# Optimization experiments

Hardware: AMD Instinct MI355X
Metric: run time of the kernel (lower is better)

The kernel has to match this reference:

```python
import math
import jax, jax.numpy as jnp
import numpy as np

DIM_Q = 1024
DIM_K = 1024
DIM_V = 1024
NUM_HEADS = 16
B, NQ, NK = 4, 1024, 1024
LN_EPS = 1e-5


def setup_inputs() -> dict:
    key = jax.random.key(0)
    ks = jax.random.split(key, 16)
    s = lambda fan_in: 1.0 / math.sqrt(fan_in)
    inp = {
        "Q": jax.random.normal(ks[0], (B, NQ, DIM_Q), dtype=jnp.float32),
        "K": jax.random.normal(ks[1], (B, NK, DIM_K), dtype=jnp.float32),
        # attention projections (nn.Linear: weight [out, in])
        "Wq": jax.random.uniform(ks[2], (DIM_V, DIM_Q), jnp.float32, -s(DIM_Q), s(DIM_Q)),
        "bq": jax.random.uniform(ks[3], (DIM_V,), jnp.float32, -s(DIM_Q), s(DIM_Q)),
        "Wk": jax.random.uniform(ks[4], (DIM_V, DIM_K), jnp.float32, -s(DIM_K), s(DIM_K)),
        "bk": jax.random.uniform(ks[5], (DIM_V,), jnp.float32, -s(DIM_K), s(DIM_K)),
        "Wv": jax.random.uniform(ks[6], (DIM_V, DIM_K), jnp.float32, -s(DIM_K), s(DIM_K)),
        "bv": jax.random.uniform(ks[7], (DIM_V,), jnp.float32, -s(DIM_K), s(DIM_K)),
        # LayerNorms
        "ln0_g": jnp.ones((DIM_V,), jnp.float32),
        "ln0_b": jnp.zeros((DIM_V,), jnp.float32),
        "ln1_g": jnp.ones((DIM_V,), jnp.float32),
        "ln1_b": jnp.zeros((DIM_V,), jnp.float32),
        # SwiGLU: w12 [2*hidden, in], w3 [out, hidden], hidden = out = DIM_V
        "W12": jax.random.uniform(ks[8], (2 * DIM_V, DIM_V), jnp.float32, -s(DIM_V), s(DIM_V)),
        "b12": jax.random.uniform(ks[9], (2 * DIM_V,), jnp.float32, -s(DIM_V), s(DIM_V)),
        "W3": jax.random.uniform(ks[10], (DIM_V, DIM_V), jnp.float32, -s(DIM_V), s(DIM_V)),
        "b3": jax.random.uniform(ks[11], (DIM_V,), jnp.float32, -s(DIM_V), s(DIM_V)),
    }
    return inp


def _layernorm(x, g, b):
    mu = jnp.mean(x, axis=-1, keepdims=True)
    var = jnp.mean(jnp.square(x - mu), axis=-1, keepdims=True)
    return (x - mu) * jax.lax.rsqrt(var + LN_EPS) * g + b


def reference(Q, K, Wq, bq, Wk, bk, Wv, bv, ln0_g, ln0_b, ln1_g, ln1_b, W12, b12, W3, b3):
    H = NUM_HEADS
    dh = DIM_V // H
    Qp = jnp.einsum("bnd,vd->bnv", Q, Wq) + bq   # [B,NQ,DIM_V]
    Kp = jnp.einsum("bnd,vd->bnv", K, Wk) + bk   # [B,NK,DIM_V]
    Vp = jnp.einsum("bnd,vd->bnv", K, Wv) + bv
    # torch.cat(x.split(dh, 2), 0) => layout [H*B, N, dh] with head index major
    Qh = Qp.reshape(B, NQ, H, dh).transpose(2, 0, 1, 3)  # [H,B,NQ,dh]
    Kh = Kp.reshape(B, NK, H, dh).transpose(2, 0, 1, 3)
    Vh = Vp.reshape(B, NK, H, dh).transpose(2, 0, 1, 3)
    # NOTE: original scales by sqrt(dim_V), not sqrt(head_dim)
    scores = jnp.einsum("hbqd,hbkd->hbqk", Qh, Kh) / math.sqrt(DIM_V)
    A = jax.nn.softmax(scores, axis=-1)                  # [H,B,NQ,NK]
    Oh = Qh + jnp.einsum("hbqk,hbkd->hbqd", A, Vh)       # residual pre-concat
    O = Oh.transpose(1, 2, 0, 3).reshape(B, NQ, DIM_V)
    O = _layernorm(O, ln0_g, ln0_b)
    # SwiGLU FFN
    x12 = jnp.einsum("bnd,hd->bnh", O, W12) + b12
    x1, x2 = jnp.split(x12, 2, axis=-1)
    O = O + (jnp.einsum("bnh,oh->bno", jax.nn.silu(x1) * x2, W3) + b3)
    O = _layernorm(O, ln1_g, ln1_b)
    return O, A.reshape(H * B, NQ, NK)
```

## Files before the change

### kernel.cpp

```cpp
#include <hip/hip_runtime.h>
#include <math.h>

#define BATCH 4
#define NQL   1024
#define NKL   1024
#define DIM   1024
#define NHEAD 16
#define DHEAD 64
#define SCALE 0.03125f

typedef float  f32x4  __attribute__((ext_vector_type(4)));
typedef short  short8 __attribute__((ext_vector_type(8)));

__device__ __forceinline__ ushort f2bf(float x) {
    uint u = __float_as_uint(x);
    u += 0x7FFFu + ((u >> 16) & 1u);
    return (ushort)(u >> 16);
}
__device__ __forceinline__ float bf2f(ushort h) {
    return __uint_as_float(((uint)h) << 16);
}

__global__ __launch_bounds__(256)
void split_bf(const float* __restrict__ x, ushort* __restrict__ hi,
              ushort* __restrict__ lo, int n4)
{
    const int i = blockIdx.x * 256 + threadIdx.x;
    if (i >= n4) return;
    const float4 v = ((const float4*)x)[i];
    ushort4 h, l;
    h.x = f2bf(v.x); l.x = f2bf(v.x - bf2f(h.x));
    h.y = f2bf(v.y); l.y = f2bf(v.y - bf2f(h.y));
    h.z = f2bf(v.z); l.z = f2bf(v.z - bf2f(h.z));
    h.w = f2bf(v.w); l.w = f2bf(v.w - bf2f(h.w));
    ((ushort4*)hi)[i] = h;
    ((ushort4*)lo)[i] = l;
}

#define LDK 40

template<int NPROD, int BIAS, int RESID, int OMODE>
__global__ __launch_bounds__(256)
void gemm_mfma(const ushort* __restrict__ Ahi, const ushort* __restrict__ Alo,
               int lda,
               const ushort* __restrict__ Bhi, const ushort* __restrict__ Blo,
               int ldb,
               const float* __restrict__ bias,
               const float* __restrict__ rm,
               float* __restrict__ Cm, ushort* __restrict__ Chi,
               int ldc, int Kd, float scale)
{
    constexpr int NT_ = (NPROD == 3) ? 4 : 2;
    __shared__ ushort lds[2][NT_][128 * LDK];

    const int tid  = threadIdx.x;
    const int lane = tid & 63;
    const int wid  = tid >> 6;
    const int wr   = wid >> 1, wc = wid & 1;
    const int bm   = blockIdx.x * 128;
    const int bn   = blockIdx.y * 128;

    const ushort* tb[NT_];
    int tldv[NT_];
    tb[0] = Ahi + (size_t)bm * lda;  tldv[0] = lda;
    tb[1] = Bhi + (size_t)bn * ldb;  tldv[1] = ldb;
    if constexpr (NPROD == 3) {
        tb[2] = Alo + (size_t)bm * lda;  tldv[2] = lda;
        tb[3] = Blo + (size_t)bn * ldb;  tldv[3] = ldb;
    }

    int4 rg[NT_][2];
    auto gload = [&](int k0) {
#pragma unroll
        for (int tt = 0; tt < NT_; ++tt)
#pragma unroll
            for (int p = 0; p < 2; ++p) {
                const int idx = p * 256 + tid;
                rg[tt][p] = *(const int4*)(tb[tt] + (size_t)(idx >> 2) * tldv[tt]
                                           + k0 + ((idx & 3) << 3));
            }
    };
    auto dswrite = [&](int buf) {
#pragma unroll
        for (int tt = 0; tt < NT_; ++tt)
#pragma unroll
            for (int p = 0; p < 2; ++p) {
                const int idx = p * 256 + tid;
                *(int4*)&lds[buf][tt][(idx >> 2) * LDK + ((idx & 3) << 3)] = rg[tt][p];
            }
    };

    gload(0);
    dswrite(0);
    __syncthreads();

    f32x4 acc[4][4] = {};
    int cur = 0;
    const int nt = Kd >> 5;

    const int rA = wr * 64 + (lane & 15);
    const int rB = wc * 64 + (lane & 15);
    const int kg = (lane >> 4) << 3;

    for (int t = 0; t < nt; ++t) {
        const bool more = (t + 1) < nt;
        if (more) gload((t + 1) << 5);

        short8 ah[4], bh[4], al[4], bl[4];
#pragma unroll
        for (int f = 0; f < 4; ++f) {
            ah[f] = *(const short8*)&lds[cur][0][(rA + f * 16) * LDK + kg];
            bh[f] = *(const short8*)&lds[cur][1][(rB + f * 16) * LDK + kg];
        }
        if constexpr (NPROD == 3) {
#pragma unroll
            for (int f = 0; f < 4; ++f) {
                al[f] = *(const short8*)&lds[cur][2][(rA + f * 16) * LDK + kg];
                bl[f] = *(const short8*)&lds[cur][3][(rB + f * 16) * LDK + kg];
            }
        }

#pragma unroll
        for (int fi = 0; fi < 4; ++fi)
#pragma unroll
            for (int fj = 0; fj < 4; ++fj) {
                acc[fi][fj] = __builtin_amdgcn_mfma_f32_16x16x32_bf16(ah[fi], bh[fj], acc[fi][fj], 0, 0, 0);
                if constexpr (NPROD == 3) {
                    acc[fi][fj] = __builtin_amdgcn_mfma_f32_16x16x32_bf16(ah[fi], bl[fj], acc[fi][fj], 0, 0, 0);
                    acc[fi][fj] = __builtin_amdgcn_mfma_f32_16x16x32_bf16(al[fi], bh[fj], acc[fi][fj], 0, 0, 0);
                }
            }

        if (more) dswrite(cur ^ 1);
        __syncthreads();
        cur ^= 1;
    }

    float biasv[4];
    if (BIAS) {
#pragma unroll
        for (int fj = 0; fj < 4; ++fj)
            biasv[fj] = bias[bn + wc * 64 + fj * 16 + (lane & 15)];
    }
#pragma unroll
    for (int fi = 0; fi < 4; ++fi) {
        const int r0 = bm + wr * 64 + fi * 16 + ((lane >> 4) << 2);
#pragma unroll
        for (int fj = 0; fj < 4; ++fj) {
            const int c = bn + wc * 64 + fj * 16 + (lane & 15);
            if constexpr (OMODE == 3) {
                ushort4 v4;
#pragma unroll
                for (int r = 0; r < 4; ++r) {
                    float o = acc[fi][fj][r] * scale;
                    if (BIAS) o += biasv[fj];
                    ((ushort*)&v4)[r] = f2bf(o);
                }
                const int b   = r0 >> 10;
                const int key = r0 & 1023;
                const int h   = c >> 6;
                const int d   = c & 63;
                *(ushort4*)(Chi + ((size_t)((h << 2) + b) << 16) + (size_t)d * 1024 + key) = v4;
            } else {
#pragma unroll
                for (int r = 0; r < 4; ++r) {
                    float o = acc[fi][fj][r] * scale;
                    if (BIAS) o += biasv[fj];
                    if (RESID) o += rm[(size_t)(r0 + r) * ldc + c];
                    if (OMODE == 0 || OMODE == 1)
                        Cm[(size_t)(r0 + r) * ldc + c] = o;
                    if (OMODE == 1 || OMODE == 2)
                        Chi[(size_t)(r0 + r) * ldc + c] = f2bf(o);
                }
            }
        }
    }
}

__global__ __launch_bounds__(256)
void flash_attn(const ushort* __restrict__ QpHi,
                const ushort* __restrict__ KpHi,
                const ushort* __restrict__ Vt,
                const float*  __restrict__ Qp,
                float* __restrict__ Aout,
                float* __restrict__ Oa)
{
    __shared__ ushort Ks[2][64][72];
    __shared__ ushort Vs[2][64][72];
    __shared__ ushort Ps[4][32][72];

    const int tid  = threadIdx.x;
    const int lane = tid & 63;
    const int w    = tid >> 6;
    const int l15  = lane & 15;
    const int lg   = lane >> 4;
    const int bm   = blockIdx.x * 128;
    const int hb   = blockIdx.y;
    const int zh   = hb >> 2, zb = hb & 3;

    const ushort* Qb  = QpHi + ((size_t)zb << 20) + zh * 64;
    const ushort* Kb  = KpHi + ((size_t)zb << 20) + zh * 64;
    const ushort* Vtb = Vt   + ((size_t)hb << 16);
    const float*  Qrb = Qp   + ((size_t)zb << 20) + zh * 64 + (size_t)bm * DIM;
    float* Ab = Aout + ((size_t)hb << 20) + (size_t)bm * NKL;
    float* Ob = Oa   + ((size_t)zb << 20) + zh * 64 + (size_t)bm * DIM;

    short8 qf[2][2];
#pragma unroll
    for (int qg = 0; qg < 2; ++qg)
#pragma unroll
        for (int kg = 0; kg < 2; ++kg)
            qf[qg][kg] = *(const short8*)(Qb + (size_t)(bm + w * 32 + qg * 16 + l15) * DIM
                                          + kg * 32 + lg * 8);

    int4 kreg[2], vreg[2];
    auto kload = [&](int kt) {
#pragma unroll
        for (int p = 0; p < 2; ++p) {
            const int c = p * 256 + tid;
            kreg[p] = *(const int4*)(Kb + (size_t)(kt * 64 + (c >> 3)) * DIM + (c & 7) * 8);
        }
    };
    auto kstore = [&](int buf) {
#pragma unroll
        for (int p = 0; p < 2; ++p) {
            const int c = p * 256 + tid;
            *(int4*)&Ks[buf][c >> 3][(c & 7) * 8] = kreg[p];
        }
    };
    auto vload = [&](int kt) {
#pragma unroll
        for (int p = 0; p < 2; ++p) {
            const int c = p * 256 + tid;
            vreg[p] = *(const int4*)(Vtb + (size_t)(c >> 3) * 1024 + kt * 64 + (c & 7) * 8);
        }
    };
    auto vstore = [&](int buf) {
#pragma unroll
        for (int p = 0; p < 2; ++p) {
            const int c = p * 256 + tid;
            *(int4*)&Vs[buf][c >> 3][(c & 7) * 8] = vreg[p];
        }
    };
    auto qk = [&](int buf, f32x4 (*s)[4]) {
        short8 kf[4][2];
#pragma unroll
        for (int cg = 0; cg < 4; ++cg)
#pragma unroll
            for (int kg = 0; kg < 2; ++kg)
                kf[cg][kg] = *(const short8*)&Ks[buf][cg * 16 + l15][kg * 32 + lg * 8];
#pragma unroll
        for (int qg = 0; qg < 2; ++qg)
#pragma unroll
            for (int cg = 0; cg < 4; ++cg) {
                s[qg][cg] = __builtin_amdgcn_mfma_f32_16x16x32_bf16(qf[qg][0], kf[cg][0], s[qg][cg], 0, 0, 0);
                s[qg][cg] = __builtin_amdgcn_mfma_f32_16x16x32_bf16(qf[qg][1], kf[cg][1], s[qg][cg], 0, 0, 0);
            }
    };

    float mrun[2][4], lrun[2][4];
#pragma unroll
    for (int qg = 0; qg < 2; ++qg)
#pragma unroll
        for (int r = 0; r < 4; ++r) { mrun[qg][r] = -INFINITY; lrun[qg][r] = 0.f; }

    kload(0); kstore(0); __syncthreads();
    for (int kt = 0; kt < 16; ++kt) {
        const bool more = kt < 15;
        if (more) kload(kt + 1);
        f32x4 s[2][4] = {};
        qk(kt & 1, s);
#pragma unroll
        for (int qg = 0; qg < 2; ++qg)
#pragma unroll
            for (int r = 0; r < 4; ++r) {
                const float v0 = s[qg][0][r] * SCALE, v1 = s[qg][1][r] * SCALE;
                const float v2 = s[qg][2][r] * SCALE, v3 = s[qg][3][r] * SCALE;
                const float tm = fmaxf(fmaxf(v0, v1), fmaxf(v2, v3));
                const float mn = fmaxf(mrun[qg][r], tm);
                const float sc = __expf(mrun[qg][r] - mn);
                lrun[qg][r] = lrun[qg][r] * sc
                            + __expf(v0 - mn) + __expf(v1 - mn)
                            + __expf(v2 - mn) + __expf(v3 - mn);
                mrun[qg][r] = mn;
            }
        if (more) { kstore((kt + 1) & 1); __syncthreads(); }
    }

    float mf[2][4], li[2][4];
#pragma unroll
    for (int qg = 0; qg < 2; ++qg)
#pragma unroll
        for (int r = 0; r < 4; ++r) {
            float m = mrun[qg][r];
#pragma unroll
            for (int off = 1; off < 16; off <<= 1) m = fmaxf(m, __shfl_xor(m, off));
            float lv = lrun[qg][r] * __expf(mrun[qg][r] - m);
#pragma unroll
            for (int off = 1; off < 16; off <<= 1) lv += __shfl_xor(lv, off);
            mf[qg][r] = m;
            li[qg][r] = 1.f / lv;
        }

    kload(0); vload(0);
    __syncthreads();
    kstore(0); vstore(0);
    __syncthreads();

    f32x4 oacc[2][4] = {};
    for (int kt = 0; kt < 16; ++kt) {
        const bool more = kt < 15;
        if (more) { kload(kt + 1); vload(kt + 1); }
        f32x4 s[2][4] = {};
        qk(kt & 1, s);

#pragma unroll
        for (int qg = 0; qg < 2; ++qg)
#pragma unroll
            for (int cg = 0; cg < 4; ++cg) {
#pragma unroll
                for (int r = 0; r < 4; ++r) {
                    const float p = __expf(s[qg][cg][r] * SCALE - mf[qg][r]) * li[qg][r];
                    Ps[w][qg * 16 + lg * 4 + r][cg * 16 + l15] = f2bf(p);
                    Ab[(size_t)(w * 32 + qg * 16 + lg * 4 + r) * NKL
                       + kt * 64 + cg * 16 + l15] = p;
                }
            }

        short8 pf[2][2], vf[4][2];
#pragma unroll
        for (int qg = 0; qg < 2; ++qg)
#pragma unroll
            for (int kk = 0; kk < 2; ++kk)
                pf[qg][kk] = *(const short8*)&Ps[w][qg * 16 + l15][kk * 32 + lg * 8];
#pragma unroll
        for (int dg = 0; dg < 4; ++dg)
#pragma unroll
            for (int kk = 0; kk < 2; ++kk)
                vf[dg][kk] = *(const short8*)&Vs[kt & 1][dg * 16 + l15][kk * 32 + lg * 8];
#pragma unroll
        for (int qg = 0; qg < 2; ++qg)
#pragma unroll
            for (int dg = 0; dg < 4; ++dg) {
                oacc[qg][dg] = __builtin_amdgcn_mfma_f32_16x16x32_bf16(pf[qg][0], vf[dg][0], oacc[qg][dg], 0, 0, 0);
                oacc[qg][dg] = __builtin_amdgcn_mfma_f32_16x16x32_bf16(pf[qg][1], vf[dg][1], oacc[qg][dg], 0, 0, 0);
            }

        if (more) { kstore((kt + 1) & 1); vstore((kt + 1) & 1); __syncthreads(); }
    }

#pragma unroll
    for (int qg = 0; qg < 2; ++qg)
#pragma unroll
        for (int dg = 0; dg < 4; ++dg)
#pragma unroll
            for (int r = 0; r < 4; ++r) {
                const size_t idx = (size_t)(w * 32 + qg * 16 + lg * 4 + r) * DIM
                                 + dg * 16 + l15;
                Ob[idx] = oacc[qg][dg][r] + Qrb[idx];
            }
}

template<int SPLIT>
__global__ __launch_bounds__(256)
void ln_rows(const float* __restrict__ in, const float* __restrict__ g,
             const float* __restrict__ b, float* __restrict__ out,
             ushort* __restrict__ ohi, ushort* __restrict__ olo)
{
    const int row = blockIdx.x;
    const int tid = threadIdx.x;
    const float4 xv = *(const float4*)(in + (size_t)row * DIM + (tid << 2));

    float s = xv.x + xv.y + xv.z + xv.w;
    float q = xv.x * xv.x + xv.y * xv.y + xv.z * xv.z + xv.w * xv.w;
#pragma unroll
    for (int off = 32; off; off >>= 1) {
        s += __shfl_xor(s, off);
        q += __shfl_xor(q, off);
    }
    __shared__ float ss[4], qq[4];
    if ((tid & 63) == 0) { ss[tid >> 6] = s; qq[tid >> 6] = q; }
    __syncthreads();
    s = ss[0] + ss[1] + ss[2] + ss[3];
    q = qq[0] + qq[1] + qq[2] + qq[3];

    const float mu  = s * (1.f / 1024.f);
    const float var = q * (1.f / 1024.f) - mu * mu;
    const float rs  = rsqrtf(var + 1e-5f);

    const float4 gv = *(const float4*)(g + (tid << 2));
    const float4 bv = *(const float4*)(b + (tid << 2));
    float4 o;
    o.x = (xv.x - mu) * rs * gv.x + bv.x;
    o.y = (xv.y - mu) * rs * gv.y + bv.y;
    o.z = (xv.z - mu) * rs * gv.z + bv.z;
    o.w = (xv.w - mu) * rs * gv.w + bv.w;
    *(float4*)(out + (size_t)row * DIM + (tid << 2)) = o;

    if (SPLIT) {
        ushort4 h, l;
        h.x = f2bf(o.x); l.x = f2bf(o.x - bf2f(h.x));
        h.y = f2bf(o.y); l.y = f2bf(o.y - bf2f(h.y));
        h.z = f2bf(o.z); l.z = f2bf(o.z - bf2f(h.z));
        h.w = f2bf(o.w); l.w = f2bf(o.w - bf2f(h.w));
        ((ushort4*)(ohi + (size_t)row * DIM))[tid] = h;
        ((ushort4*)(olo + (size_t)row * DIM))[tid] = l;
    }
}

__global__ __launch_bounds__(256)
void silu_mul(const float* __restrict__ x12, ushort* __restrict__ ghi,
              ushort* __restrict__ glo)
{
    const int i = blockIdx.x * 256 + threadIdx.x;
    const int n = i >> 8;
    const int c = (i & 255) << 2;
    const float4 a = *(const float4*)(x12 + (size_t)n * 2048 + c);
    const float4 b = *(const float4*)(x12 + (size_t)n * 2048 + 1024 + c);
    float4 o;
    o.x = a.x / (1.f + __expf(-a.x)) * b.x;
    o.y = a.y / (1.f + __expf(-a.y)) * b.y;
    o.z = a.z / (1.f + __expf(-a.z)) * b.z;
    o.w = a.w / (1.f + __expf(-a.w)) * b.w;
    ushort4 h, l;
    h.x = f2bf(o.x); l.x = f2bf(o.x - bf2f(h.x));
    h.y = f2bf(o.y); l.y = f2bf(o.y - bf2f(h.y));
    h.z = f2bf(o.z); l.z = f2bf(o.z - bf2f(h.z));
    h.w = f2bf(o.w); l.w = f2bf(o.w - bf2f(h.w));
    ((ushort4*)ghi)[i] = h;
    ((ushort4*)glo)[i] = l;
}

extern "C" void kernel_launch(void* const* d_in, const int* in_sizes, int n_in,
                              void* d_out, int out_size, void* d_ws, size_t ws_size,
                              hipStream_t stream)
{
    const float* Q   = (const float*)d_in[0];
    const float* K   = (const float*)d_in[1];
    const float* Wq  = (const float*)d_in[2];
    const float* bq  = (const float*)d_in[3];
    const float* Wk  = (const float*)d_in[4];
    const float* bk  = (const float*)d_in[5];
    const float* Wv  = (const float*)d_in[6];
    const float* bv  = (const float*)d_in[7];
    const float* g0  = (const float*)d_in[8];
    const float* be0 = (const float*)d_in[9];
    const float* g1  = (const float*)d_in[10];
    const float* be1 = (const float*)d_in[11];
    const float* W12 = (const float*)d_in[12];
    const float* b12 = (const float*)d_in[13];
    const float* W3  = (const float*)d_in[14];
    const float* b3  = (const float*)d_in[15];

    float* ws   = (float*)d_ws;
    float* Qp   = ws;
    float* Oa   = ws + (1u << 22);
    float* Oln  = ws + (2u << 22);
    float* x12  = ws + (3u << 22);

    ushort* wsm   = (ushort*)(ws + (3u << 22));
    ushort* Wqhi  = wsm;
    ushort* Wqlo  = wsm + (1u << 20);
    ushort* Wkhi  = wsm + (2u << 20);
    ushort* Wklo  = wsm + (3u << 20);
    ushort* Wvhi  = wsm + (4u << 20);
    ushort* Wvlo  = wsm + (5u << 20);

    ushort* u     = (ushort*)(ws + (5u << 22));
    ushort* QpHi  = u;
    ushort* KpHi  = u + (1u << 22);
    ushort* Qhi   = u + (2u << 22);
    ushort* Qlo   = u + (3u << 22);
    ushort* Khi   = u + (4u << 22);
    ushort* Klo   = u + (5u << 22);
    ushort* Vt    = u + (6u << 22);
    ushort* OlnHi = Qhi;
    ushort* OlnLo = Qlo;
    ushort* GHi   = Khi;
    ushort* GLo   = Klo;
    ushort* W12hi = u + (7u << 22);
    ushort* W12lo = W12hi + (1u << 21);
    ushort* W3hi  = W12hi + (2u << 21);
    ushort* W3lo  = W12hi + (3u << 21);

    float* Oout = (float*)d_out;
    float* Aout = Oout + (1u << 22);

    const dim3 blk(256);

    split_bf<<<4096, blk, 0, stream>>>(Q,   Qhi,   Qlo,   1 << 20);
    split_bf<<<4096, blk, 0, stream>>>(K,   Khi,   Klo,   1 << 20);
    split_bf<<<1024, blk, 0, stream>>>(Wq,  Wqhi,  Wqlo,  1 << 18);
    split_bf<<<1024, blk, 0, stream>>>(Wk,  Wkhi,  Wklo,  1 << 18);
    split_bf<<<1024, blk, 0, stream>>>(Wv,  Wvhi,  Wvlo,  1 << 18);
    split_bf<<<2048, blk, 0, stream>>>(W12, W12hi, W12lo, 1 << 19);
    split_bf<<<1024, blk, 0, stream>>>(W3,  W3hi,  W3lo,  1 << 18);

    gemm_mfma<3,1,0,1><<<dim3(32,8), blk, 0, stream>>>(
        Qhi, Qlo, DIM, Wqhi, Wqlo, DIM, bq, nullptr, Qp, QpHi, DIM, DIM, 1.f);
    gemm_mfma<3,1,0,2><<<dim3(32,8), blk, 0, stream>>>(
        Khi, Klo, DIM, Wkhi, Wklo, DIM, bk, nullptr, nullptr, KpHi, DIM, DIM, 1.f);
    gemm_mfma<3,1,0,3><<<dim3(32,8), blk, 0, stream>>>(
        Khi, Klo, DIM, Wvhi, Wvlo, DIM, bv, nullptr, nullptr, Vt, DIM, DIM, 1.f);

    flash_attn<<<dim3(8,64), blk, 0, stream>>>(QpHi, KpHi, Vt, Qp, Aout, Oa);

    ln_rows<1><<<4096, blk, 0, stream>>>(Oa, g0, be0, Oln, OlnHi, OlnLo);

    gemm_mfma<3,1,0,0><<<dim3(32,16), blk, 0, stream>>>(
        OlnHi, OlnLo, DIM, W12hi, W12lo, DIM, b12, nullptr, x12, nullptr, 2048, DIM, 1.f);

    silu_mul<<<4096, blk, 0, stream>>>(x12, GHi, GLo);

    gemm_mfma<3,1,1,0><<<dim3(32,8), blk, 0, stream>>>(
        GHi, GLo, DIM, W3hi, W3lo, DIM, b3, Oln, Oa, nullptr, DIM, DIM, 1.f);

    ln_rows<0><<<4096, blk, 0, stream>>>(Oa, g1, be1, Oout, nullptr, nullptr);
}
```

Before: 979.3 us.

## Shrink GEMM tiles to 64x64 and stream the three split-bf16 products sequentially

Reworks the split-bf16 GEMM to use 64x64 output tiles with a K-step of 64, and runs the hi*hi, hi*lo and lo*hi products as consecutive K-passes instead of interleaving them per tile. This cuts LDS and register use and quadruples the grid so more blocks fit per CU (launch bounds ask for 4). In exchange, each loaded element is reused less, so global and LDS traffic per FLOP rise and the A/B tiles are fetched three times over.

```diff
diff --git a/kernel.cpp b/kernel.cpp
--- a/kernel.cpp
+++ b/kernel.cpp
@@ -37,10 +37,10 @@
     ((ushort4*)lo)[i] = l;
 }
 
-#define LDK 40
+#define LDK2 72
 
 template<int NPROD, int BIAS, int RESID, int OMODE>
-__global__ __launch_bounds__(256)
+__global__ __launch_bounds__(256, 4)
 void gemm_mfma(const ushort* __restrict__ Ahi, const ushort* __restrict__ Alo,
                int lda,
                const ushort* __restrict__ Bhi, const ushort* __restrict__ Blo,
@@ -50,85 +50,72 @@
                float* __restrict__ Cm, ushort* __restrict__ Chi,
                int ldc, int Kd, float scale)
 {
-    constexpr int NT_ = (NPROD == 3) ? 4 : 2;
-    __shared__ ushort lds[2][NT_][128 * LDK];
+    __shared__ ushort As_[2][64 * LDK2];
+    __shared__ ushort Bs_[2][64 * LDK2];
 
     const int tid  = threadIdx.x;
     const int lane = tid & 63;
     const int wid  = tid >> 6;
     const int wr   = wid >> 1, wc = wid & 1;
-    const int bm   = blockIdx.x * 128;
-    const int bn   = blockIdx.y * 128;
-
-    const ushort* tb[NT_];
-    int tldv[NT_];
-    tb[0] = Ahi + (size_t)bm * lda;  tldv[0] = lda;
-    tb[1] = Bhi + (size_t)bn * ldb;  tldv[1] = ldb;
-    if constexpr (NPROD == 3) {
-        tb[2] = Alo + (size_t)bm * lda;  tldv[2] = lda;
-        tb[3] = Blo + (size_t)bn * ldb;  tldv[3] = ldb;
-    }
-
-    int4 rg[NT_][2];
-    auto gload = [&](int k0) {
-#pragma unroll
-        for (int tt = 0; tt < NT_; ++tt)
-#pragma unroll
-            for (int p = 0; p < 2; ++p) {
-                const int idx = p * 256 + tid;
-                rg[tt][p] = *(const int4*)(tb[tt] + (size_t)(idx >> 2) * tldv[tt]
-                                           + k0 + ((idx & 3) << 3));
-            }
+    const int l15  = lane & 15;
+    const int lg   = lane >> 4;
+    const int bm   = blockIdx.x * 64;
+    const int bn   = blockIdx.y * 64;
+
+    const int tpp = Kd >> 6;
+    const int nt  = NPROD * tpp;
+
+    int4 ra[2], rb[2];
+    auto gload = [&](int t) {
+        const ushort* Asrc = Ahi;
+        const ushort* Bsrc = Bhi;
+        int tt = t;
+        if constexpr (NPROD == 3) {
+            if (t >= 2 * tpp)  { Asrc = Alo; tt = t - 2 * tpp; }
+            else if (t >= tpp) { Bsrc = Blo; tt = t - tpp; }
+        }
+        const int k0 = tt << 6;
+#pragma unroll
+        for (int p = 0; p < 2; ++p) {
+            const int idx = p * 256 + tid;
+            const int row = idx >> 3, col = (idx & 7) << 3;
+            ra[p] = *(const int4*)(Asrc + (size_t)(bm + row) * lda + k0 + col);
+            rb[p] = *(const int4*)(Bsrc + (size_t)(bn + row) * ldb + k0 + col);
+        }
     };
     auto dswrite = [&](int buf) {
 #pragma unroll
-        for (int tt = 0; tt < NT_; ++tt)
-#pragma unroll
-            for (int p = 0; p < 2; ++p) {
-                const int idx = p * 256 + tid;
-                *(int4*)&lds[buf][tt][(idx >> 2) * LDK + ((idx & 3) << 3)] = rg[tt][p];
-            }
-    };
-
-    gload(0);
-    dswrite(0);
-    __syncthreads();
-
-    f32x4 acc[4][4] = {};
+        for (int p = 0; p < 2; ++p) {
+            const int idx = p * 256 + tid;
+            const int row = idx >> 3, col = (idx & 7) << 3;
+            *(int4*)&As_[buf][row * LDK2 + col] = ra[p];
+            *(int4*)&Bs_[buf][row * LDK2 + col] = rb[p];
+        }
+    };
+
+    gload(0); dswrite(0); __syncthreads();
+
+    f32x4 acc[2][2] = {};
     int cur = 0;
-    const int nt = Kd >> 5;
-
-    const int rA = wr * 64 + (lane & 15);
-    const int rB = wc * 64 + (lane & 15);
-    const int kg = (lane >> 4) << 3;
 
     for (int t = 0; t < nt; ++t) {
         const bool more = (t + 1) < nt;
-        if (more) gload((t + 1) << 5);
-
-        short8 ah[4], bh[4], al[4], bl[4];
-#pragma unroll
-        for (int f = 0; f < 4; ++f) {
-            ah[f] = *(const short8*)&lds[cur][0][(rA + f * 16) * LDK + kg];
-            bh[f] = *(const short8*)&lds[cur][1][(rB + f * 16) * LDK + kg];
-        }
-        if constexpr (NPROD == 3) {
-#pragma unroll
-            for (int f = 0; f < 4; ++f) {
-                al[f] = *(const short8*)&lds[cur][2][(rA + f * 16) * LDK + kg];
-                bl[f] = *(const short8*)&lds[cur][3][(rB + f * 16) * LDK + kg];
-            }
-        }
-
-#pragma unroll
-        for (int fi = 0; fi < 4; ++fi)
-#pragma unroll
-            for (int fj = 0; fj < 4; ++fj) {
-                acc[fi][fj] = __builtin_amdgcn_mfma_f32_16x16x32_bf16(ah[fi], bh[fj], acc[fi][fj], 0, 0, 0);
-                if constexpr (NPROD == 3) {
-                    acc[fi][fj] = __builtin_amdgcn_mfma_f32_16x16x32_bf16(ah[fi], bl[fj], acc[fi][fj], 0, 0, 0);
-                    acc[fi][fj] = __builtin_amdgcn_mfma_f32_16x16x32_bf16(al[fi], bh[fj], acc[fi][fj], 0, 0, 0);
-                }
+        if (more) gload(t + 1);
+
+        short8 ah[2][2], bh[2][2];
+#pragma unroll
+        for (int f = 0; f < 2; ++f)
+#pragma unroll
+            for (int ks = 0; ks < 2; ++ks) {
+                ah[f][ks] = *(const short8*)&As_[cur][(wr * 32 + f * 16 + l15) * LDK2 + ks * 32 + lg * 8];
+                bh[f][ks] = *(const short8*)&Bs_[cur][(wc * 32 + f * 16 + l15) * LDK2 + ks * 32 + lg * 8];
+            }
+#pragma unroll
+        for (int fi = 0; fi < 2; ++fi)
+#pragma unroll
+            for (int fj = 0; fj < 2; ++fj) {
+                acc[fi][fj] = __builtin_amdgcn_mfma_f32_16x16x32_bf16(ah[fi][0], bh[fj][0], acc[fi][fj], 0, 0, 0);
+                acc[fi][fj] = __builtin_amdgcn_mfma_f32_16x16x32_bf16(ah[fi][1], bh[fj][1], acc[fi][fj], 0, 0, 0);
             }
 
         if (more) dswrite(cur ^ 1);
@@ -136,18 +123,18 @@
         cur ^= 1;
     }
 
-    float biasv[4];
+    float biasv[2];
     if (BIAS) {
 #pragma unroll
-        for (int fj = 0; fj < 4; ++fj)
-            biasv[fj] = bias[bn + wc * 64 + fj * 16 + (lane & 15)];
-    }
-#pragma unroll
-    for (int fi = 0; fi < 4; ++fi) {
-        const int r0 = bm + wr * 64 + fi * 16 + ((lane >> 4) << 2);
-#pragma unroll
-        for (int fj = 0; fj < 4; ++fj) {
-            const int c = bn + wc * 64 + fj * 16 + (lane & 15);
+        for (int fj = 0; fj < 2; ++fj)
+            biasv[fj] = bias[bn + wc * 32 + fj * 16 + l15];
+    }
+#pragma unroll
+    for (int fi = 0; fi < 2; ++fi) {
+        const int r0 = bm + wr * 32 + fi * 16 + (lg << 2);
+#pragma unroll
+        for (int fj = 0; fj < 2; ++fj) {
+            const int c = bn + wc * 32 + fj * 16 + l15;
             if constexpr (OMODE == 3) {
                 ushort4 v4;
 #pragma unroll
@@ -496,23 +483,23 @@
     split_bf<<<2048, blk, 0, stream>>>(W12, W12hi, W12lo, 1 << 19);
     split_bf<<<1024, blk, 0, stream>>>(W3,  W3hi,  W3lo,  1 << 18);
 
-    gemm_mfma<3,1,0,1><<<dim3(32,8), blk, 0, stream>>>(
+    gemm_mfma<3,1,0,1><<<dim3(64,16), blk, 0, stream>>>(
         Qhi, Qlo, DIM, Wqhi, Wqlo, DIM, bq, nullptr, Qp, QpHi, DIM, DIM, 1.f);
-    gemm_mfma<3,1,0,2><<<dim3(32,8), blk, 0, stream>>>(
+    gemm_mfma<3,1,0,2><<<dim3(64,16), blk, 0, stream>>>(
         Khi, Klo, DIM, Wkhi, Wklo, DIM, bk, nullptr, nullptr, KpHi, DIM, DIM, 1.f);
-    gemm_mfma<3,1,0,3><<<dim3(32,8), blk, 0, stream>>>(
+    gemm_mfma<3,1,0,3><<<dim3(64,16), blk, 0, stream>>>(
         Khi, Klo, DIM, Wvhi, Wvlo, DIM, bv, nullptr, nullptr, Vt, DIM, DIM, 1.f);
 
     flash_attn<<<dim3(8,64), blk, 0, stream>>>(QpHi, KpHi, Vt, Qp, Aout, Oa);
 
     ln_rows<1><<<4096, blk, 0, stream>>>(Oa, g0, be0, Oln, OlnHi, OlnLo);
 
-    gemm_mfma<3,1,0,0><<<dim3(32,16), blk, 0, stream>>>(
+    gemm_mfma<3,1,0,0><<<dim3(64,32), blk, 0, stream>>>(
         OlnHi, OlnLo, DIM, W12hi, W12lo, DIM, b12, nullptr, x12, nullptr, 2048, DIM, 1.f);
 
     silu_mul<<<4096, blk, 0, stream>>>(x12, GHi, GLo);
 
-    gemm_mfma<3,1,1,0><<<dim3(32,8), blk, 0, stream>>>(
+    gemm_mfma<3,1,1,0><<<dim3(64,16), blk, 0, stream>>>(
         GHi, GLo, DIM, W3hi, W3lo, DIM, b3, Oln, Oa, nullptr, DIM, DIM, 1.f);
 
     ln_rows<0><<<4096, blk, 0, stream>>>(Oa, g1, be1, Oout, nullptr, nullptr);
```

Result: slower. 1.699 ms (+73.5%).
